# Performance work log

Measured on AMD Instinct MI355X. Metric: run time of the kernel, lower is better.

## Reference

```python
import jax, jax.numpy as jnp
import numpy as np

B, N, C, H, KS = 4, 1024, 768, 12, 7
DFF = 4 * C
HD = C // H
EPS = 1e-5


def layernorm(x, g, b):
    mu = jnp.mean(x, axis=-1, keepdims=True)
    var = jnp.mean(jnp.square(x - mu), axis=-1, keepdims=True)
    return (x - mu) * jax.lax.rsqrt(var + EPS) * g + b


def setup_inputs() -> dict:
    key = jax.random.key(0)
    ks = jax.random.split(key, 16)
    s = 0.02
    return {
        "x": jax.random.normal(ks[0], (B, N, C), jnp.float32),
        "w_qkv": jax.random.normal(ks[1], (3 * C, C), jnp.float32) * s,
        "b_qkv": jnp.zeros((3 * C,), jnp.float32),
        "w_proj": jax.random.normal(ks[2], (C, C), jnp.float32) * s,
        "b_proj": jnp.zeros((C,), jnp.float32),
        "w_fc1": jax.random.normal(ks[3], (DFF, C), jnp.float32) * s,
        "b_fc1": jnp.zeros((DFF,), jnp.float32),
        "w_fc2": jax.random.normal(ks[4], (C, DFF), jnp.float32) * s,
        "b_fc2": jnp.zeros((C,), jnp.float32),
        "t_before": jnp.eye(H, dtype=jnp.float32) + s * jax.random.normal(ks[5], (H, H), jnp.float32),
        "t_after": jnp.eye(H, dtype=jnp.float32) + s * jax.random.normal(ks[6], (H, H), jnp.float32),
        "g1": jnp.ones((C,), jnp.float32), "be1": jnp.zeros((C,), jnp.float32),
        "g2": jnp.ones((C,), jnp.float32), "be2": jnp.zeros((C,), jnp.float32),
        "dw_w": jax.random.normal(ks[7], (C, 1, KS), jnp.float32) * s,
        "dw_b": jnp.zeros((C,), jnp.float32),
        "gm": jnp.ones((C,), jnp.float32), "bm": jnp.zeros((C,), jnp.float32),
    }


def reference(x, w_qkv, b_qkv, w_proj, b_proj, w_fc1, b_fc1, w_fc2, b_fc2,
              t_before, t_after, g1, be1, g2, be2, dw_w, dw_b, gm, bm):
    residual = x
    h = layernorm(x, g1, be1)
    qkv = h @ w_qkv.T + b_qkv                       # [B,N,3C]
    qkv = qkv.reshape(B, N, 3, H, HD).transpose(2, 0, 3, 1, 4)  # [3,B,H,N,HD]
    q, k, v = qkv[0], qkv[1], qkv[2]
    scale = HD ** -0.5
    attn = jnp.einsum('bhnd,bhmd->bhnm', q, k) * scale          # [B,H,N,N]
    # head mixing before softmax: attn_perm @ T_before.T over head dim
    attn = jnp.einsum('bhnm,gh->bgnm', attn, t_before)
    attn = jax.nn.softmax(attn, axis=-1)
    # head mixing after softmax
    attn = jnp.einsum('bhnm,gh->bgnm', attn, t_after)
    out = jnp.einsum('bhnm,bhmd->bhnd', attn, v)                 # [B,H,N,HD]
    out = out.transpose(0, 2, 1, 3).reshape(B, N, C)
    out = out @ w_proj.T + b_proj
    x = residual + out
    residual = x
    h = layernorm(x, g2, be2)
    # MLP transform: depthwise conv1d over tokens + layernorm
    ht = h.transpose(0, 2, 1)                                    # [B,C,N]
    ht = jax.lax.conv_general_dilated(
        ht, dw_w, window_strides=(1,), padding=[(KS // 2, KS // 2)],
        feature_group_count=C, dimension_numbers=('NCH', 'OIH', 'NCH'))
    ht = ht + dw_b[None, :, None]
    h = layernorm(ht.transpose(0, 2, 1), gm, bm)
    # standard MLP (fc1 -> GELU -> fc2)
    h = jax.nn.gelu(h @ w_fc1.T + b_fc1, approximate=False)
    h = h @ w_fc2.T + b_fc2
    return residual + h
```

## Files before the change

### kernel.cpp

```cpp
#include <hip/hip_runtime.h>


typedef unsigned short u16;
typedef __bf16 bf16x8 __attribute__((ext_vector_type(8)));
typedef float f32x4 __attribute__((ext_vector_type(4)));

using gvoid = __attribute__((address_space(1))) const void;
using lvoid = __attribute__((address_space(3))) void;
#define GLD16(GP, LP) __builtin_amdgcn_global_load_lds((gvoid*)(GP), (lvoid*)(LP), 16, 0, 0)

__device__ __forceinline__ u16 f2b(float f) {
  unsigned u = __float_as_uint(f);
  u = (u + 0x7FFFu + ((u >> 16) & 1u)) >> 16;
  return (u16)u;
}
__device__ __forceinline__ float b2f(u16 b) { return __uint_as_float(((unsigned)b) << 16); }
__device__ __forceinline__ float gelu_exact(float x) {
  return 0.5f * x * (1.f + erff(x * 0.70710678118654752f));
}

__global__ void cast_f2b(const float* __restrict__ in, u16* __restrict__ out, int n) {
  int i = blockIdx.x * 256 + threadIdx.x;
  if (i < n) out[i] = f2b(in[i]);
}

template <typename OutT>
__global__ __launch_bounds__(256) void ln_row(const float* __restrict__ x,
                                              const float* __restrict__ g,
                                              const float* __restrict__ be,
                                              OutT* __restrict__ out) {
  const long row = blockIdx.x;
  const float* xr = x + row * 768;
  OutT* yr = out + row * 768;
  const int tid = threadIdx.x;
  const int w = tid >> 6, lane = tid & 63;
  float v[3], s = 0.f, s2 = 0.f;
#pragma unroll
  for (int i = 0; i < 3; ++i) {
    v[i] = xr[tid + i * 256];
    s += v[i];
    s2 += v[i] * v[i];
  }
#pragma unroll
  for (int off = 32; off; off >>= 1) {
    s += __shfl_xor(s, off);
    s2 += __shfl_xor(s2, off);
  }
  __shared__ float red[8];
  if (lane == 0) { red[w] = s; red[w + 4] = s2; }
  __syncthreads();
  s = red[0] + red[1] + red[2] + red[3];
  s2 = red[4] + red[5] + red[6] + red[7];
  const float mu = s * (1.f / 768.f);
  const float var = s2 * (1.f / 768.f) - mu * mu;
  const float rstd = rsqrtf(var + 1e-5f);
#pragma unroll
  for (int i = 0; i < 3; ++i) {
    const int c = tid + i * 256;
    float y = (v[i] - mu) * rstd * g[c] + be[c];
    if constexpr (sizeof(OutT) == 2) yr[c] = f2b(y);
    else yr[c] = y;
  }
}

template <int ZMODE, int ACT, bool HAS_RES, typename OutT>
__global__ __launch_bounds__(256, 2) void gemm_bt(
    const u16* __restrict__ Abase, const u16* __restrict__ Bbase, OutT* __restrict__ Cbase,
    const float* __restrict__ bias, const float* __restrict__ res,
    int M, int N, int K, int lda, int ldb, int ldc, int ldr, float scale) {
  __shared__ __align__(16) u16 As[128 * 32];
  __shared__ __align__(16) u16 Bs[128 * 32];
  const int tid = threadIdx.x;
  const int w = tid >> 6, lane = tid & 63;
  const int z = blockIdx.z;
  long aoff = 0, boff = 0, coff = 0;
  if (ZMODE == 1) {
    const int b = z / 12, h = z % 12;
    aoff = (long)b * 1024 * 2304 + h * 64;
    boff = aoff + 768;
    coff = (long)z * 1024 * 1024;
  }
  const u16* A = Abase + aoff;
  const u16* B = Bbase + boff;
  OutT* C = Cbase + coff;

  const long rowA = (long)blockIdx.y * 128;
  const long colB = (long)blockIdx.x * 128;

  f32x4 acc[4][4];
#pragma unroll
  for (int m = 0; m < 4; ++m)
#pragma unroll
    for (int n = 0; n < 4; ++n) acc[m][n] = f32x4{0.f, 0.f, 0.f, 0.f};

  const int wr = w >> 1, wc = w & 1;
  const int l16 = lane & 15, lh = lane >> 4;
  const int srow = tid >> 2;
  const int scol = (tid & 3) * 8;

  for (int k0 = 0; k0 < K; k0 += 32) {
#pragma unroll
    for (int r = 0; r < 2; ++r) {
      GLD16(A + (rowA + r * 64 + srow) * (long)lda + k0 + scol, &As[r * 2048 + w * 512]);
      GLD16(B + (colB + r * 64 + srow) * (long)ldb + k0 + scol, &Bs[r * 2048 + w * 512]);
    }
    __syncthreads();
    bf16x8 a[4], bb[4];
#pragma unroll
    for (int m = 0; m < 4; ++m)
      a[m] = *reinterpret_cast<const bf16x8*>(&As[(wr * 64 + m * 16 + l16) * 32 + lh * 8]);
#pragma unroll
    for (int n = 0; n < 4; ++n)
      bb[n] = *reinterpret_cast<const bf16x8*>(&Bs[(wc * 64 + n * 16 + l16) * 32 + lh * 8]);
#pragma unroll
    for (int m = 0; m < 4; ++m)
#pragma unroll
      for (int n = 0; n < 4; ++n)
        acc[m][n] = __builtin_amdgcn_mfma_f32_16x16x32_bf16(a[m], bb[n], acc[m][n], 0, 0, 0);
    __syncthreads();
  }

  const long row0 = rowA + wr * 64;
  const long col0 = colB + wc * 64;
#pragma unroll
  for (int m = 0; m < 4; ++m)
#pragma unroll
    for (int n = 0; n < 4; ++n)
#pragma unroll
      for (int r = 0; r < 4; ++r) {
        const long row = row0 + m * 16 + lh * 4 + r;
        const long col = col0 + n * 16 + l16;
        float v = acc[m][n][r] * scale;
        if (bias) v += bias[col];
        if (ACT == 1) v = gelu_exact(v);
        if (HAS_RES) v += res[row * (long)ldr + col];
        if constexpr (sizeof(OutT) == 2) C[row * (long)ldc + col] = f2b(v);
        else C[row * (long)ldc + col] = v;
      }
}

__global__ __launch_bounds__(256) void mix_heads(u16* __restrict__ attn,
                                                 const float* __restrict__ T) {
  __shared__ float Ts[144];
  const int tid = threadIdx.x;
  if (tid < 144) Ts[tid] = T[tid];
  __syncthreads();
  const long gid = (long)blockIdx.x * 256 + tid;
  const int b = (int)(gid >> 20);
  const long base = ((long)b * 12 << 20) | (gid & 0xFFFFF);
  float s[12];
#pragma unroll
  for (int h = 0; h < 12; ++h) s[h] = b2f(attn[base + ((long)h << 20)]);
#pragma unroll
  for (int g = 0; g < 12; ++g) {
    float o = 0.f;
#pragma unroll
    for (int h = 0; h < 12; ++h) o += Ts[g * 12 + h] * s[h];
    attn[base + ((long)g << 20)] = f2b(o);
  }
}

__global__ __launch_bounds__(256) void softmax_rows(u16* __restrict__ attn) {
  u16* p = attn + (long)blockIdx.x * 1024;
  const int tid = threadIdx.x;
  const int w = tid >> 6, lane = tid & 63;
  float v[4];
  float mx = -1e30f;
#pragma unroll
  for (int i = 0; i < 4; ++i) {
    v[i] = b2f(p[tid + i * 256]);
    mx = fmaxf(mx, v[i]);
  }
#pragma unroll
  for (int off = 32; off; off >>= 1) mx = fmaxf(mx, __shfl_xor(mx, off));
  __shared__ float red[8];
  if (lane == 0) red[w] = mx;
  __syncthreads();
  mx = fmaxf(fmaxf(red[0], red[1]), fmaxf(red[2], red[3]));
  float s = 0.f;
#pragma unroll
  for (int i = 0; i < 4; ++i) {
    v[i] = __expf(v[i] - mx);
    s += v[i];
  }
#pragma unroll
  for (int off = 32; off; off >>= 1) s += __shfl_xor(s, off);
  if (lane == 0) red[w + 4] = s;
  __syncthreads();
  s = red[4] + red[5] + red[6] + red[7];
  const float inv = 1.f / s;
#pragma unroll
  for (int i = 0; i < 4; ++i) p[tid + i * 256] = f2b(v[i] * inv);
}

__global__ __launch_bounds__(256, 2) void av_gemm(const u16* __restrict__ attn,
                                                  const u16* __restrict__ qkv,
                                                  u16* __restrict__ out) {
  __shared__ __align__(16) u16 As[128 * 32];
  __shared__ __align__(16) u16 Vt[64 * 40];
  const int tid = threadIdx.x;
  const int w = tid >> 6, lane = tid & 63;
  const int z = blockIdx.y;
  const int b = z / 12, h = z % 12;
  const u16* A = attn + (long)z * 1024 * 1024;
  const u16* V = qkv + (long)b * 1024 * 2304 + 1536 + h * 64;
  const long rowA = (long)blockIdx.x * 128;

  f32x4 acc[2][4];
#pragma unroll
  for (int m = 0; m < 2; ++m)
#pragma unroll
    for (int n = 0; n < 4; ++n) acc[m][n] = f32x4{0.f, 0.f, 0.f, 0.f};

  const int l16 = lane & 15, lh = lane >> 4;
  const int srow = tid >> 2;
  const int scol = (tid & 3) * 8;

  for (int k0 = 0; k0 < 1024; k0 += 32) {
#pragma unroll
    for (int r = 0; r < 2; ++r)
      GLD16(A + (rowA + r * 64 + srow) * 1024 + k0 + scol, &As[r * 2048 + w * 512]);
#pragma unroll
    for (int i = 0; i < 8; ++i) {
      const int idx = i * 256 + tid;
      const int kk = idx >> 6, d = idx & 63;
      Vt[d * 40 + kk] = V[(long)(k0 + kk) * 2304 + d];
    }
    __syncthreads();
    bf16x8 a[2], bv[4];
#pragma unroll
    for (int m = 0; m < 2; ++m)
      a[m] = *reinterpret_cast<const bf16x8*>(&As[(w * 32 + m * 16 + l16) * 32 + lh * 8]);
#pragma unroll
    for (int n = 0; n < 4; ++n)
      bv[n] = *reinterpret_cast<const bf16x8*>(&Vt[(n * 16 + l16) * 40 + lh * 8]);
#pragma unroll
    for (int m = 0; m < 2; ++m)
#pragma unroll
      for (int n = 0; n < 4; ++n)
        acc[m][n] = __builtin_amdgcn_mfma_f32_16x16x32_bf16(a[m], bv[n], acc[m][n], 0, 0, 0);
    __syncthreads();
  }
  const long row0 = rowA + w * 32;
#pragma unroll
  for (int m = 0; m < 2; ++m)
#pragma unroll
    for (int n = 0; n < 4; ++n)
#pragma unroll
      for (int r = 0; r < 4; ++r) {
        const long tok = row0 + m * 16 + lh * 4 + r;
        const int d = n * 16 + l16;
        out[((long)b * 1024 + tok) * 768 + h * 64 + d] = f2b(acc[m][n][r]);
      }
}

__global__ __launch_bounds__(256) void dwconv(const float* __restrict__ h2,
                                              const float* __restrict__ wgt,
                                              const float* __restrict__ bias,
                                              float* __restrict__ ct) {
  const long gid = (long)blockIdx.x * 256 + threadIdx.x;
  const int c = (int)(gid % 768);
  const int n = (int)((gid / 768) % 1024);
  const int b = (int)(gid / (768 * 1024));
  float acc = bias[c];
#pragma unroll
  for (int t = 0; t < 7; ++t) {
    const int nn = n + t - 3;
    if (nn >= 0 && nn < 1024) acc += h2[((long)b * 1024 + nn) * 768 + c] * wgt[c * 7 + t];
  }
  ct[gid] = acc;
}

extern "C" void kernel_launch(void* const* d_in, const int* in_sizes, int n_in,
                              void* d_out, int out_size, void* d_ws, size_t ws_size,
                              hipStream_t stream) {
  const float* x      = (const float*)d_in[0];
  const float* w_qkv  = (const float*)d_in[1];
  const float* b_qkv  = (const float*)d_in[2];
  const float* w_proj = (const float*)d_in[3];
  const float* b_proj = (const float*)d_in[4];
  const float* w_fc1  = (const float*)d_in[5];
  const float* b_fc1  = (const float*)d_in[6];
  const float* w_fc2  = (const float*)d_in[7];
  const float* b_fc2  = (const float*)d_in[8];
  const float* t_bef  = (const float*)d_in[9];
  const float* t_aft  = (const float*)d_in[10];
  const float* g1     = (const float*)d_in[11];
  const float* be1    = (const float*)d_in[12];
  const float* g2     = (const float*)d_in[13];
  const float* be2    = (const float*)d_in[14];
  const float* dw_w   = (const float*)d_in[15];
  const float* dw_b   = (const float*)d_in[16];
  const float* gm     = (const float*)d_in[17];
  const float* bm     = (const float*)d_in[18];
  float* out = (float*)d_out;

  char* wsp = (char*)d_ws;
  size_t off = 0;
  auto alloc = [&](size_t bytes) {
    char* r = wsp + off;
    off += (bytes + 255) & ~(size_t)255;
    return r;
  };
  u16* wqkv_b  = (u16*)alloc((size_t)2304 * 768 * 2);
  u16* wproj_b = (u16*)alloc((size_t)768 * 768 * 2);
  u16* wfc1_b  = (u16*)alloc((size_t)3072 * 768 * 2);
  u16* wfc2_b  = (u16*)alloc((size_t)768 * 3072 * 2);
  u16* h1      = (u16*)alloc((size_t)4096 * 768 * 2);
  u16* attn_out = h1;
  u16* qkvb    = (u16*)alloc((size_t)4096 * 2304 * 2);
  char* attn_region = alloc((size_t)48 * 1024 * 1024 * 2);
  u16* attn = (u16*)attn_region;
  size_t ro = 0;
  auto ralloc = [&](size_t bytes) {
    char* r = attn_region + ro;
    ro += (bytes + 255) & ~(size_t)255;
    return r;
  };
  float* x2   = (float*)ralloc((size_t)4096 * 768 * 4);
  float* h2   = (float*)ralloc((size_t)4096 * 768 * 4);
  float* ct   = (float*)ralloc((size_t)4096 * 768 * 4);
  u16*   hm   = (u16*)ralloc((size_t)4096 * 768 * 2);
  u16*   fc1o = (u16*)ralloc((size_t)4096 * 3072 * 2);
  (void)ws_size; (void)n_in; (void)in_sizes; (void)out_size;

  cast_f2b<<<(2304 * 768 + 255) / 256, 256, 0, stream>>>(w_qkv, wqkv_b, 2304 * 768);
  cast_f2b<<<(768 * 768 + 255) / 256, 256, 0, stream>>>(w_proj, wproj_b, 768 * 768);
  cast_f2b<<<(3072 * 768 + 255) / 256, 256, 0, stream>>>(w_fc1, wfc1_b, 3072 * 768);
  cast_f2b<<<(768 * 3072 + 255) / 256, 256, 0, stream>>>(w_fc2, wfc2_b, 768 * 3072);

  ln_row<u16><<<4096, 256, 0, stream>>>(x, g1, be1, h1);
  gemm_bt<0, 0, false, u16><<<dim3(18, 32, 1), 256, 0, stream>>>(
      h1, wqkv_b, qkvb, b_qkv, nullptr, 4096, 2304, 768, 768, 768, 2304, 0, 1.f);
  gemm_bt<1, 0, false, u16><<<dim3(8, 8, 48), 256, 0, stream>>>(
      qkvb, qkvb, attn, nullptr, nullptr, 1024, 1024, 64, 2304, 2304, 1024, 0, 0.125f);
  mix_heads<<<16384, 256, 0, stream>>>(attn, t_bef);
  softmax_rows<<<48 * 1024, 256, 0, stream>>>(attn);
  mix_heads<<<16384, 256, 0, stream>>>(attn, t_aft);
  av_gemm<<<dim3(8, 48), 256, 0, stream>>>(attn, qkvb, attn_out);
  gemm_bt<0, 0, true, float><<<dim3(6, 32, 1), 256, 0, stream>>>(
      attn_out, wproj_b, x2, b_proj, x, 4096, 768, 768, 768, 768, 768, 768, 1.f);
  ln_row<float><<<4096, 256, 0, stream>>>(x2, g2, be2, h2);
  dwconv<<<(4096 * 768) / 256, 256, 0, stream>>>(h2, dw_w, dw_b, ct);
  ln_row<u16><<<4096, 256, 0, stream>>>(ct, gm, bm, hm);
  gemm_bt<0, 1, false, u16><<<dim3(24, 32, 1), 256, 0, stream>>>(
      hm, wfc1_b, fc1o, b_fc1, nullptr, 4096, 3072, 768, 768, 768, 3072, 0, 1.f);
  gemm_bt<0, 0, true, float><<<dim3(6, 32, 1), 256, 0, stream>>>(
      fc1o, wfc2_b, out, b_fc2, x2, 4096, 768, 3072, 3072, 3072, 768, 768, 1.f);
}
```

Before: 531.0 us.

## Fuse attention scores with head mixing, fuse softmax with post-mix, double-buffer GEMMs

```diff
diff --git a/kernel.cpp b/kernel.cpp
--- a/kernel.cpp
+++ b/kernel.cpp
@@ -3,6 +3,7 @@
 
 typedef unsigned short u16;
 typedef __bf16 bf16x8 __attribute__((ext_vector_type(8)));
+typedef u16 u16x8 __attribute__((ext_vector_type(8)));
 typedef float f32x4 __attribute__((ext_vector_type(4)));
 
 using gvoid = __attribute__((address_space(1))) const void;
@@ -19,9 +20,24 @@
   return 0.5f * x * (1.f + erff(x * 0.70710678118654752f));
 }
 
-__global__ void cast_f2b(const float* __restrict__ in, u16* __restrict__ out, int n) {
-  int i = blockIdx.x * 256 + threadIdx.x;
-  if (i < n) out[i] = f2b(in[i]);
+__global__ __launch_bounds__(256) void cast_all(const float* __restrict__ s0,
+                                                const float* __restrict__ s1,
+                                                const float* __restrict__ s2,
+                                                const float* __restrict__ s3,
+                                                u16* __restrict__ d0, u16* __restrict__ d1,
+                                                u16* __restrict__ d2, u16* __restrict__ d3) {
+  const int n0 = 1769472 / 4, n1 = 589824 / 4, n2 = 2359296 / 4;
+  int j = blockIdx.x * 256 + threadIdx.x;
+  const float* src;
+  u16* dst;
+  if (j < n0) { src = s0; dst = d0; }
+  else if ((j -= n0) < n1) { src = s1; dst = d1; }
+  else if ((j -= n1) < n2) { src = s2; dst = d2; }
+  else { j -= n2; src = s3; dst = d3; }
+  const float4 v = ((const float4*)src)[j];
+  ushort4 o;
+  o.x = f2b(v.x); o.y = f2b(v.y); o.z = f2b(v.z); o.w = f2b(v.w);
+  ((ushort4*)dst)[j] = o;
 }
 
 template <typename OutT>
@@ -63,74 +79,71 @@
   }
 }
 
-template <int ZMODE, int ACT, bool HAS_RES, typename OutT>
-__global__ __launch_bounds__(256, 2) void gemm_bt(
-    const u16* __restrict__ Abase, const u16* __restrict__ Bbase, OutT* __restrict__ Cbase,
+template <int TM, int TN, int ACT, bool HAS_RES, typename OutT>
+__global__ __launch_bounds__(256) void gemm_bt(
+    const u16* __restrict__ A, const u16* __restrict__ B, OutT* __restrict__ C,
     const float* __restrict__ bias, const float* __restrict__ res,
-    int M, int N, int K, int lda, int ldb, int ldc, int ldr, float scale) {
-  __shared__ __align__(16) u16 As[128 * 32];
-  __shared__ __align__(16) u16 Bs[128 * 32];
+    int K, int lda, int ldb, int ldc, int ldr) {
+  constexpr int WM = TM / 2, WN = TN / 2, MR = WM / 16, NR = WN / 16;
+  __shared__ __align__(16) u16 As[2][TM * 32];
+  __shared__ __align__(16) u16 Bs[2][TN * 32];
   const int tid = threadIdx.x;
   const int w = tid >> 6, lane = tid & 63;
-  const int z = blockIdx.z;
-  long aoff = 0, boff = 0, coff = 0;
-  if (ZMODE == 1) {
-    const int b = z / 12, h = z % 12;
-    aoff = (long)b * 1024 * 2304 + h * 64;
-    boff = aoff + 768;
-    coff = (long)z * 1024 * 1024;
-  }
-  const u16* A = Abase + aoff;
-  const u16* B = Bbase + boff;
-  OutT* C = Cbase + coff;
-
-  const long rowA = (long)blockIdx.y * 128;
-  const long colB = (long)blockIdx.x * 128;
-
-  f32x4 acc[4][4];
-#pragma unroll
-  for (int m = 0; m < 4; ++m)
-#pragma unroll
-    for (int n = 0; n < 4; ++n) acc[m][n] = f32x4{0.f, 0.f, 0.f, 0.f};
-
   const int wr = w >> 1, wc = w & 1;
   const int l16 = lane & 15, lh = lane >> 4;
+  const long rowA = (long)blockIdx.y * TM;
+  const long colB = (long)blockIdx.x * TN;
   const int srow = tid >> 2;
-  const int scol = (tid & 3) * 8;
-
-  for (int k0 = 0; k0 < K; k0 += 32) {
-#pragma unroll
-    for (int r = 0; r < 2; ++r) {
-      GLD16(A + (rowA + r * 64 + srow) * (long)lda + k0 + scol, &As[r * 2048 + w * 512]);
-      GLD16(B + (colB + r * 64 + srow) * (long)ldb + k0 + scol, &Bs[r * 2048 + w * 512]);
-    }
-    __syncthreads();
-    bf16x8 a[4], bb[4];
-#pragma unroll
-    for (int m = 0; m < 4; ++m)
-      a[m] = *reinterpret_cast<const bf16x8*>(&As[(wr * 64 + m * 16 + l16) * 32 + lh * 8]);
-#pragma unroll
-    for (int n = 0; n < 4; ++n)
-      bb[n] = *reinterpret_cast<const bf16x8*>(&Bs[(wc * 64 + n * 16 + l16) * 32 + lh * 8]);
-#pragma unroll
-    for (int m = 0; m < 4; ++m)
-#pragma unroll
-      for (int n = 0; n < 4; ++n)
+  const int scol = (((tid & 3) ^ (srow & 3))) * 8;
+
+  f32x4 acc[MR][NR];
+#pragma unroll
+  for (int m = 0; m < MR; ++m)
+#pragma unroll
+    for (int n = 0; n < NR; ++n) acc[m][n] = f32x4{0.f, 0.f, 0.f, 0.f};
+
+  auto stage = [&](int buf, int k0) {
+#pragma unroll
+    for (int r = 0; r < TM / 64; ++r)
+      GLD16(A + (rowA + r * 64 + srow) * (long)lda + k0 + scol, (char*)As[buf] + r * 4096 + w * 1024);
+#pragma unroll
+    for (int r = 0; r < TN / 64; ++r)
+      GLD16(B + (colB + r * 64 + srow) * (long)ldb + k0 + scol, (char*)Bs[buf] + r * 4096 + w * 1024);
+  };
+
+  stage(0, 0);
+  __syncthreads();
+  const int nk = K >> 5;
+  const int rx = (lh ^ (l16 & 3)) * 8;
+  for (int t = 0; t < nk; ++t) {
+    const int buf = t & 1;
+    if (t + 1 < nk) stage(buf ^ 1, (t + 1) << 5);
+    bf16x8 a[MR], bb[NR];
+#pragma unroll
+    for (int m = 0; m < MR; ++m)
+      a[m] = *(const bf16x8*)&As[buf][(wr * WM + m * 16 + l16) * 32 + rx];
+#pragma unroll
+    for (int n = 0; n < NR; ++n)
+      bb[n] = *(const bf16x8*)&Bs[buf][(wc * WN + n * 16 + l16) * 32 + rx];
+#pragma unroll
+    for (int m = 0; m < MR; ++m)
+#pragma unroll
+      for (int n = 0; n < NR; ++n)
         acc[m][n] = __builtin_amdgcn_mfma_f32_16x16x32_bf16(a[m], bb[n], acc[m][n], 0, 0, 0);
     __syncthreads();
   }
 
-  const long row0 = rowA + wr * 64;
-  const long col0 = colB + wc * 64;
-#pragma unroll
-  for (int m = 0; m < 4; ++m)
-#pragma unroll
-    for (int n = 0; n < 4; ++n)
+  const long row0 = rowA + wr * WM;
+  const long col0 = colB + wc * WN;
+#pragma unroll
+  for (int m = 0; m < MR; ++m)
+#pragma unroll
+    for (int n = 0; n < NR; ++n)
 #pragma unroll
       for (int r = 0; r < 4; ++r) {
         const long row = row0 + m * 16 + lh * 4 + r;
         const long col = col0 + n * 16 + l16;
-        float v = acc[m][n][r] * scale;
+        float v = acc[m][n][r];
         if (bias) v += bias[col];
         if (ACT == 1) v = gelu_exact(v);
         if (HAS_RES) v += res[row * (long)ldr + col];
@@ -139,136 +152,187 @@
       }
 }
 
-__global__ __launch_bounds__(256) void mix_heads(u16* __restrict__ attn,
-                                                 const float* __restrict__ T) {
+__global__ __launch_bounds__(256) void scores_mix(const u16* __restrict__ qkv,
+                                                  const float* __restrict__ Tb,
+                                                  u16* __restrict__ attn) {
+  __shared__ __align__(16) u16 Qs[32 * 768];
+  __shared__ __align__(16) u16 Ks[32 * 768];
   __shared__ float Ts[144];
   const int tid = threadIdx.x;
-  if (tid < 144) Ts[tid] = T[tid];
+  const int w = tid >> 6, lane = tid & 63;
+  const int b = blockIdx.z;
+  const int n0 = blockIdx.y * 32, m0 = blockIdx.x * 32;
+  if (tid < 144) Ts[tid] = Tb[tid];
+  const char* qb = (const char*)qkv;
+#pragma unroll
+  for (int i = 0; i < 12; ++i) {
+    const int idx = i * 256 + tid;
+    const int r = idx / 96, t = idx % 96;
+    const int s = t ^ (r & 7);
+    const long rQ = ((long)b * 1024 + n0 + r) * 4608;
+    const long rK = ((long)b * 1024 + m0 + r) * 4608;
+    GLD16(qb + rQ + s * 16, (char*)Qs + (i * 256 + w * 64) * 16);
+    GLD16(qb + rK + 1536 + s * 16, (char*)Ks + (i * 256 + w * 64) * 16);
+  }
   __syncthreads();
-  const long gid = (long)blockIdx.x * 256 + tid;
-  const int b = (int)(gid >> 20);
-  const long base = ((long)b * 12 << 20) | (gid & 0xFFFFF);
-  float s[12];
-#pragma unroll
-  for (int h = 0; h < 12; ++h) s[h] = b2f(attn[base + ((long)h << 20)]);
+  const int wr = w >> 1, wc = w & 1;
+  const int l16 = lane & 15, lh = lane >> 4;
+  const int x7 = l16 & 7;
+  const char* Qrow = (const char*)Qs + (wr * 16 + l16) * 1536;
+  const char* Krow = (const char*)Ks + (wc * 16 + l16) * 1536;
+  f32x4 acc[12];
+#pragma unroll
+  for (int h = 0; h < 12; ++h) acc[h] = f32x4{0.f, 0.f, 0.f, 0.f};
+#pragma unroll
+  for (int h = 0; h < 12; ++h)
+#pragma unroll
+    for (int kk = 0; kk < 2; ++kk) {
+      const int slot = h * 8 + kk * 4 + lh;
+      const bf16x8 a = *(const bf16x8*)(Qrow + (slot ^ x7) * 16);
+      const bf16x8 bb = *(const bf16x8*)(Krow + (slot ^ x7) * 16);
+      acc[h] = __builtin_amdgcn_mfma_f32_16x16x32_bf16(a, bb, acc[h], 0, 0, 0);
+    }
 #pragma unroll
   for (int g = 0; g < 12; ++g) {
-    float o = 0.f;
-#pragma unroll
-    for (int h = 0; h < 12; ++h) o += Ts[g * 12 + h] * s[h];
-    attn[base + ((long)g << 20)] = f2b(o);
-  }
-}
-
-__global__ __launch_bounds__(256) void softmax_rows(u16* __restrict__ attn) {
-  u16* p = attn + (long)blockIdx.x * 1024;
+    f32x4 o = f32x4{0.f, 0.f, 0.f, 0.f};
+#pragma unroll
+    for (int h = 0; h < 12; ++h) o += Ts[g * 12 + h] * acc[h];
+    u16* dst = attn + (((long)(b * 12 + g)) << 20) +
+               (long)(n0 + wr * 16 + lh * 4) * 1024 + (m0 + wc * 16 + l16);
+#pragma unroll
+    for (int r = 0; r < 4; ++r) dst[r * 1024] = f2b(o[r] * 0.125f);
+  }
+}
+
+__global__ __launch_bounds__(256) void softmax_mix(u16* __restrict__ attn,
+                                                   const float* __restrict__ Tg) {
+  const int bi = blockIdx.x >> 10;
+  const int n = blockIdx.x & 1023;
+  __shared__ float Ta[144];
+  __shared__ float red[8];
   const int tid = threadIdx.x;
   const int w = tid >> 6, lane = tid & 63;
-  float v[4];
-  float mx = -1e30f;
-#pragma unroll
-  for (int i = 0; i < 4; ++i) {
-    v[i] = b2f(p[tid + i * 256]);
-    mx = fmaxf(mx, v[i]);
-  }
-#pragma unroll
-  for (int off = 32; off; off >>= 1) mx = fmaxf(mx, __shfl_xor(mx, off));
-  __shared__ float red[8];
-  if (lane == 0) red[w] = mx;
-  __syncthreads();
-  mx = fmaxf(fmaxf(red[0], red[1]), fmaxf(red[2], red[3]));
-  float s = 0.f;
-#pragma unroll
-  for (int i = 0; i < 4; ++i) {
-    v[i] = __expf(v[i] - mx);
-    s += v[i];
-  }
-#pragma unroll
-  for (int off = 32; off; off >>= 1) s += __shfl_xor(s, off);
-  if (lane == 0) red[w + 4] = s;
-  __syncthreads();
-  s = red[4] + red[5] + red[6] + red[7];
-  const float inv = 1.f / s;
-#pragma unroll
-  for (int i = 0; i < 4; ++i) p[tid + i * 256] = f2b(v[i] * inv);
-}
-
-__global__ __launch_bounds__(256, 2) void av_gemm(const u16* __restrict__ attn,
-                                                  const u16* __restrict__ qkv,
-                                                  u16* __restrict__ out) {
-  __shared__ __align__(16) u16 As[128 * 32];
-  __shared__ __align__(16) u16 Vt[64 * 40];
+  if (tid < 144) Ta[tid] = Tg[tid];
+  const long base = (((long)bi * 12) << 20) + (long)n * 1024;
+  float p[12][4];
+#pragma unroll
+  for (int h = 0; h < 12; ++h) {
+    const uint2 d = ((const uint2*)(attn + base + ((long)h << 20)))[tid];
+    float v[4] = {b2f((u16)(d.x & 0xffff)), b2f((u16)(d.x >> 16)),
+                  b2f((u16)(d.y & 0xffff)), b2f((u16)(d.y >> 16))};
+    float mx = fmaxf(fmaxf(v[0], v[1]), fmaxf(v[2], v[3]));
+#pragma unroll
+    for (int off = 32; off; off >>= 1) mx = fmaxf(mx, __shfl_xor(mx, off));
+    __syncthreads();
+    if (lane == 0) red[w] = mx;
+    __syncthreads();
+    mx = fmaxf(fmaxf(red[0], red[1]), fmaxf(red[2], red[3]));
+    float s = 0.f;
+#pragma unroll
+    for (int i = 0; i < 4; ++i) {
+      v[i] = __expf(v[i] - mx);
+      s += v[i];
+    }
+#pragma unroll
+    for (int off = 32; off; off >>= 1) s += __shfl_xor(s, off);
+    if (lane == 0) red[w + 4] = s;
+    __syncthreads();
+    s = red[4] + red[5] + red[6] + red[7];
+    const float inv = 1.f / s;
+#pragma unroll
+    for (int i = 0; i < 4; ++i) p[h][i] = v[i] * inv;
+  }
+#pragma unroll
+  for (int g = 0; g < 12; ++g) {
+    float o[4] = {0.f, 0.f, 0.f, 0.f};
+#pragma unroll
+    for (int h = 0; h < 12; ++h) {
+      const float t = Ta[g * 12 + h];
+#pragma unroll
+      for (int i = 0; i < 4; ++i) o[i] += t * p[h][i];
+    }
+    uint2 d;
+    d.x = (unsigned)f2b(o[0]) | ((unsigned)f2b(o[1]) << 16);
+    d.y = (unsigned)f2b(o[2]) | ((unsigned)f2b(o[3]) << 16);
+    ((uint2*)(attn + base + ((long)g << 20)))[tid] = d;
+  }
+}
+
+__global__ __launch_bounds__(256) void av_gemm(const u16* __restrict__ attn,
+                                               const u16* __restrict__ qkv,
+                                               u16* __restrict__ out) {
+  __shared__ __align__(16) u16 As[2][64 * 32];
+  __shared__ __align__(16) u16 Vt[2][64 * 40];
   const int tid = threadIdx.x;
   const int w = tid >> 6, lane = tid & 63;
-  const int z = blockIdx.y;
-  const int b = z / 12, h = z % 12;
-  const u16* A = attn + (long)z * 1024 * 1024;
+  const int z = blockIdx.y, b = z / 12, h = z % 12;
+  const u16* A = attn + ((long)z << 20);
   const u16* V = qkv + (long)b * 1024 * 2304 + 1536 + h * 64;
-  const long rowA = (long)blockIdx.x * 128;
-
-  f32x4 acc[2][4];
-#pragma unroll
-  for (int m = 0; m < 2; ++m)
-#pragma unroll
-    for (int n = 0; n < 4; ++n) acc[m][n] = f32x4{0.f, 0.f, 0.f, 0.f};
-
+  const int rowA = blockIdx.x * 64;
+  const int srow = tid >> 2;
+  const int scol = (((tid & 3) ^ (srow & 3))) * 8;
   const int l16 = lane & 15, lh = lane >> 4;
-  const int srow = tid >> 2;
-  const int scol = (tid & 3) * 8;
-
-  for (int k0 = 0; k0 < 1024; k0 += 32) {
-#pragma unroll
-    for (int r = 0; r < 2; ++r)
-      GLD16(A + (rowA + r * 64 + srow) * 1024 + k0 + scol, &As[r * 2048 + w * 512]);
-#pragma unroll
-    for (int i = 0; i < 8; ++i) {
-      const int idx = i * 256 + tid;
-      const int kk = idx >> 6, d = idx & 63;
-      Vt[d * 40 + kk] = V[(long)(k0 + kk) * 2304 + d];
-    }
+
+  f32x4 acc[4];
+#pragma unroll
+  for (int n = 0; n < 4; ++n) acc[n] = f32x4{0.f, 0.f, 0.f, 0.f};
+
+  auto stageA = [&](int buf, int k0) {
+    GLD16(A + (long)(rowA + srow) * 1024 + k0 + scol, (char*)As[buf] + w * 1024);
+  };
+  auto stageV = [&](int buf, int k0) {
+    u16x8 tmp;
+#pragma unroll
+    for (int j = 0; j < 8; ++j) tmp[j] = V[(long)(k0 + w * 8 + j) * 2304 + lane];
+    *(u16x8*)&Vt[buf][lane * 40 + w * 8] = tmp;
+  };
+
+  stageA(0, 0);
+  stageV(0, 0);
+  __syncthreads();
+  for (int t = 0; t < 32; ++t) {
+    const int buf = t & 1;
+    if (t < 31) { stageA(buf ^ 1, (t + 1) * 32); stageV(buf ^ 1, (t + 1) * 32); }
+    const bf16x8 a = *(const bf16x8*)&As[buf][(w * 16 + l16) * 32 + (lh ^ (l16 & 3)) * 8];
+    bf16x8 bv[4];
+#pragma unroll
+    for (int n = 0; n < 4; ++n)
+      bv[n] = *(const bf16x8*)&Vt[buf][(n * 16 + l16) * 40 + lh * 8];
+#pragma unroll
+    for (int n = 0; n < 4; ++n)
+      acc[n] = __builtin_amdgcn_mfma_f32_16x16x32_bf16(a, bv[n], acc[n], 0, 0, 0);
     __syncthreads();
-    bf16x8 a[2], bv[4];
-#pragma unroll
-    for (int m = 0; m < 2; ++m)
-      a[m] = *reinterpret_cast<const bf16x8*>(&As[(w * 32 + m * 16 + l16) * 32 + lh * 8]);
-#pragma unroll
-    for (int n = 0; n < 4; ++n)
-      bv[n] = *reinterpret_cast<const bf16x8*>(&Vt[(n * 16 + l16) * 40 + lh * 8]);
-#pragma unroll
-    for (int m = 0; m < 2; ++m)
-#pragma unroll
-      for (int n = 0; n < 4; ++n)
-        acc[m][n] = __builtin_amdgcn_mfma_f32_16x16x32_bf16(a[m], bv[n], acc[m][n], 0, 0, 0);
-    __syncthreads();
-  }
-  const long row0 = rowA + w * 32;
-#pragma unroll
-  for (int m = 0; m < 2; ++m)
-#pragma unroll
-    for (int n = 0; n < 4; ++n)
-#pragma unroll
-      for (int r = 0; r < 4; ++r) {
-        const long tok = row0 + m * 16 + lh * 4 + r;
-        const int d = n * 16 + l16;
-        out[((long)b * 1024 + tok) * 768 + h * 64 + d] = f2b(acc[m][n][r]);
-      }
-}
-
-__global__ __launch_bounds__(256) void dwconv(const float* __restrict__ h2,
-                                              const float* __restrict__ wgt,
-                                              const float* __restrict__ bias,
-                                              float* __restrict__ ct) {
-  const long gid = (long)blockIdx.x * 256 + threadIdx.x;
-  const int c = (int)(gid % 768);
-  const int n = (int)((gid / 768) % 1024);
-  const int b = (int)(gid / (768 * 1024));
-  float acc = bias[c];
+  }
+  const int row0 = rowA + w * 16 + lh * 4;
+#pragma unroll
+  for (int n = 0; n < 4; ++n)
+#pragma unroll
+    for (int r = 0; r < 4; ++r)
+      out[((long)b * 1024 + row0 + r) * 768 + h * 64 + n * 16 + l16] = f2b(acc[n][r]);
+}
+
+__global__ __launch_bounds__(256) void dwconv4(const float* __restrict__ h2,
+                                               const float* __restrict__ wgt,
+                                               const float* __restrict__ bias,
+                                               float* __restrict__ ct) {
+  const int idx = blockIdx.x * 256 + threadIdx.x;
+  const int c4 = idx % 192;
+  const int n = (idx / 192) % 1024;
+  const int b = idx / (192 * 1024);
+  const int c = c4 * 4;
+  float4 acc = ((const float4*)bias)[c4];
 #pragma unroll
   for (int t = 0; t < 7; ++t) {
     const int nn = n + t - 3;
-    if (nn >= 0 && nn < 1024) acc += h2[((long)b * 1024 + nn) * 768 + c] * wgt[c * 7 + t];
-  }
-  ct[gid] = acc;
+    if (nn >= 0 && nn < 1024) {
+      const float4 v = *(const float4*)&h2[((long)(b << 10) + nn) * 768 + c];
+      acc.x += v.x * wgt[(c + 0) * 7 + t];
+      acc.y += v.y * wgt[(c + 1) * 7 + t];
+      acc.z += v.z * wgt[(c + 2) * 7 + t];
+      acc.w += v.w * wgt[(c + 3) * 7 + t];
+    }
+  }
+  ((float4*)ct)[idx] = acc;
 }
 
 extern "C" void kernel_launch(void* const* d_in, const int* in_sizes, int n_in,
@@ -324,27 +388,21 @@
   u16*   fc1o = (u16*)ralloc((size_t)4096 * 3072 * 2);
   (void)ws_size; (void)n_in; (void)in_sizes; (void)out_size;
 
-  cast_f2b<<<(2304 * 768 + 255) / 256, 256, 0, stream>>>(w_qkv, wqkv_b, 2304 * 768);
-  cast_f2b<<<(768 * 768 + 255) / 256, 256, 0, stream>>>(w_proj, wproj_b, 768 * 768);
-  cast_f2b<<<(3072 * 768 + 255) / 256, 256, 0, stream>>>(w_fc1, wfc1_b, 3072 * 768);
-  cast_f2b<<<(768 * 3072 + 255) / 256, 256, 0, stream>>>(w_fc2, wfc2_b, 768 * 3072);
-
+  cast_all<<<6912, 256, 0, stream>>>(w_qkv, w_proj, w_fc1, w_fc2,
+                                     wqkv_b, wproj_b, wfc1_b, wfc2_b);
   ln_row<u16><<<4096, 256, 0, stream>>>(x, g1, be1, h1);
-  gemm_bt<0, 0, false, u16><<<dim3(18, 32, 1), 256, 0, stream>>>(
-      h1, wqkv_b, qkvb, b_qkv, nullptr, 4096, 2304, 768, 768, 768, 2304, 0, 1.f);
-  gemm_bt<1, 0, false, u16><<<dim3(8, 8, 48), 256, 0, stream>>>(
-      qkvb, qkvb, attn, nullptr, nullptr, 1024, 1024, 64, 2304, 2304, 1024, 0, 0.125f);
-  mix_heads<<<16384, 256, 0, stream>>>(attn, t_bef);
-  softmax_rows<<<48 * 1024, 256, 0, stream>>>(attn);
-  mix_heads<<<16384, 256, 0, stream>>>(attn, t_aft);
-  av_gemm<<<dim3(8, 48), 256, 0, stream>>>(attn, qkvb, attn_out);
-  gemm_bt<0, 0, true, float><<<dim3(6, 32, 1), 256, 0, stream>>>(
-      attn_out, wproj_b, x2, b_proj, x, 4096, 768, 768, 768, 768, 768, 768, 1.f);
+  gemm_bt<128, 64, 0, false, u16><<<dim3(36, 32), 256, 0, stream>>>(
+      h1, wqkv_b, qkvb, b_qkv, nullptr, 768, 768, 768, 2304, 0);
+  scores_mix<<<dim3(32, 32, 4), 256, 0, stream>>>(qkvb, t_bef, attn);
+  softmax_mix<<<4096, 256, 0, stream>>>(attn, t_aft);
+  av_gemm<<<dim3(16, 48), 256, 0, stream>>>(attn, qkvb, attn_out);
+  gemm_bt<64, 64, 0, true, float><<<dim3(12, 64), 256, 0, stream>>>(
+      attn_out, wproj_b, x2, b_proj, x, 768, 768, 768, 768, 768);
   ln_row<float><<<4096, 256, 0, stream>>>(x2, g2, be2, h2);
-  dwconv<<<(4096 * 768) / 256, 256, 0, stream>>>(h2, dw_w, dw_b, ct);
+  dwconv4<<<3072, 256, 0, stream>>>(h2, dw_w, dw_b, ct);
   ln_row<u16><<<4096, 256, 0, stream>>>(ct, gm, bm, hm);
-  gemm_bt<0, 1, false, u16><<<dim3(24, 32, 1), 256, 0, stream>>>(
-      hm, wfc1_b, fc1o, b_fc1, nullptr, 4096, 3072, 768, 768, 768, 3072, 0, 1.f);
-  gemm_bt<0, 0, true, float><<<dim3(6, 32, 1), 256, 0, stream>>>(
-      fc1o, wfc2_b, out, b_fc2, x2, 4096, 768, 3072, 3072, 3072, 768, 768, 1.f);
-}
+  gemm_bt<128, 64, 1, false, u16><<<dim3(48, 32), 256, 0, stream>>>(
+      hm, wfc1_b, fc1o, b_fc1, nullptr, 768, 768, 768, 3072, 0);
+  gemm_bt<64, 64, 0, true, float><<<dim3(12, 64), 256, 0, stream>>>(
+      fc1o, wfc2_b, out, b_fc2, x2, 3072, 3072, 3072, 768, 768);
+}
```

New measurement: 474.3 us. -10.7%, faster.
